# Optimization experiments

Measured on AMD Instinct MI355X. Metric: run time of the kernel, lower is better.

The kernel has to match this reference:

```python
import jax, jax.numpy as jnp
import numpy as np

N_STATE = 64
N_LAYERS = 3


def setup_inputs() -> dict:
    key = jax.random.key(0)
    B, L, D = 8, 8192, 64
    H = 2 * D
    ks = jax.random.split(key, 10)
    x = jax.random.normal(ks[0], (B, L, D), dtype=jnp.float32)
    W_in = jax.random.normal(ks[1], (D, H), dtype=jnp.float32) * 0.05
    b_in = jnp.zeros((H,), jnp.float32)
    # S4D parameterization: dt log-uniform in [1e-3, 1e-1], A = -0.5 + i*pi*n (S4D-Lin init)
    log_dt = jax.random.uniform(ks[2], (N_LAYERS, H), dtype=jnp.float32,
                                minval=float(np.log(1e-3)), maxval=float(np.log(1e-1)))
    log_A_real = jnp.full((N_LAYERS, H, N_STATE), float(np.log(0.5)), jnp.float32)
    A_imag = jnp.tile(jnp.pi * jnp.arange(N_STATE, dtype=jnp.float32), (N_LAYERS, H, 1))
    C_re = jax.random.normal(ks[3], (N_LAYERS, H, N_STATE), dtype=jnp.float32) * (0.5 ** 0.5)
    C_im = jax.random.normal(ks[4], (N_LAYERS, H, N_STATE), dtype=jnp.float32) * (0.5 ** 0.5)
    D_skip = jax.random.normal(ks[5], (N_LAYERS, H), dtype=jnp.float32)
    W_glu = jax.random.normal(ks[6], (N_LAYERS, 2 * H, H), dtype=jnp.float32) * 0.05
    b_glu = jnp.zeros((N_LAYERS, 2 * H), jnp.float32)
    W_out = jax.random.normal(ks[7], (H, D), dtype=jnp.float32) * 0.05
    b_out = jnp.zeros((D,), jnp.float32)
    return {"x": x, "W_in": W_in, "b_in": b_in, "log_dt": log_dt,
            "log_A_real": log_A_real, "A_imag": A_imag, "C_re": C_re, "C_im": C_im,
            "D_skip": D_skip, "W_glu": W_glu, "b_glu": b_glu,
            "W_out": W_out, "b_out": b_out}


def _s4_block(u, log_dt, log_A_real, A_imag, C_re, C_im, D_skip, W_glu, b_glu):
    # u: (B, H, L). S4D: diagonal SSM applied as a long FFT convolution.
    H, L = u.shape[1], u.shape[2]
    dt = jnp.exp(log_dt)[:, None]                       # (H,1)
    A = -jnp.exp(log_A_real) + 1j * A_imag              # (H,N), Re(A)<0 -> stable
    dtA = dt * A                                        # (H,N)
    C = (C_re + 1j * C_im) * jnp.expm1(dtA) / A         # ZOH-discretized C*B
    vand = jnp.exp(dtA[:, :, None] * jnp.arange(L, dtype=jnp.float32))  # (H,N,L)
    K = 2.0 * jnp.einsum('hn,hnl->hl', C, vand).real    # (H,L) SSM kernel
    n = 2 * L
    y = jnp.fft.irfft(jnp.fft.rfft(u, n=n) * jnp.fft.rfft(K, n=n), n=n)[..., :L]
    y = y + u * D_skip[:, None]                         # skip connection D*u
    y = jax.nn.gelu(y)
    z = jnp.einsum('bhl,gh->bgl', y, W_glu) + b_glu[None, :, None]  # pointwise H->2H
    a, g = jnp.split(z, 2, axis=1)
    return a * jax.nn.sigmoid(g)                        # GLU


def _rmsnorm(x):
    # F.normalize(x, dim=-1) * sqrt(dim)
    scale = jnp.sqrt(jnp.asarray(x.shape[-1], jnp.float32))
    nrm = jnp.linalg.norm(x, axis=-1, keepdims=True)
    return x / jnp.maximum(nrm, 1e-12) * scale


def reference(x, W_in, b_in, log_dt, log_A_real, A_imag, C_re, C_im,
              D_skip, W_glu, b_glu, W_out, b_out):
    h = x @ W_in + b_in                                 # (B,L,H)
    for i in range(N_LAYERS):
        u = h.swapaxes(-1, -2)                          # (B,H,L)
        y = _s4_block(u, log_dt[i], log_A_real[i], A_imag[i], C_re[i], C_im[i],
                      D_skip[i], W_glu[i], b_glu[i]).swapaxes(-1, -2)
        h = _rmsnorm(y + h)                             # PreNormResidual
    return h @ W_out + b_out
```

## Files before the change

### kernel.cpp

```cpp
#include <hip/hip_runtime.h>
#include <math.h>

#define BB 8
#define LL 8192
#define DD 64
#define HH 128
#define NN 64
#define NLAYER 3
#define LC 64
#define NC 128
#define LST 137
#define SIS 136

typedef _Float16 half_t;
typedef _Float16 f16x8_t __attribute__((ext_vector_type(8)));
typedef _Float16 f16x4_t __attribute__((ext_vector_type(4)));
typedef _Float16 f16x2_t __attribute__((ext_vector_type(2)));
typedef float    f32x4_t __attribute__((ext_vector_type(4)));

#define SZ_WB   ((size_t)HH*NN*2)
#define SZ_WGT  ((size_t)NLAYER*256*HH/2)
#define SZ_WOT  ((size_t)DD*HH/2)
#define SZ_WIT  ((size_t)HH*DD/2)
#define SZ_AM   ((size_t)HH*64*192/2)
#define SZ_HT   ((size_t)BB*HH*LL/2)
#define SZ_YT   ((size_t)BB*HH*LL/2)

__global__ __launch_bounds__(256) void kPrep(const float* __restrict__ logdt,
   const float* __restrict__ logA, const float* __restrict__ Aim,
   const float* __restrict__ Cre, const float* __restrict__ Cim,
   const float* __restrict__ Wglu, const float* __restrict__ Wout,
   const float* __restrict__ Win,
   float* __restrict__ wb3, float* __restrict__ wl3, half_t* __restrict__ Amat3,
   half_t* __restrict__ wgt, half_t* __restrict__ woT, half_t* __restrict__ wiT) {
  __shared__ float  ktap[4][64];
  __shared__ half_t gst[4][64][128];
  int bid = blockIdx.x;
  int t = threadIdx.x;
  if (bid < 96) {
    int layer = bid >> 5;
    int blk   = bid & 31;
    float* wb = wb3 + (size_t)layer*SZ_WB;
    float* wl = wl3 + (size_t)layer*SZ_WB;
    half_t* Amat = Amat3 + (size_t)layer*HH*64*192;
    int w = t >> 6;
    int n = t & 63;
    int h = blk*4 + w;
    float dt = expf(logdt[layer*HH + h]);
    int idx = (layer*HH + h)*NN + n;
    float ar = -expf(logA[idx]);
    float ai = Aim[idx];
    float er = expf(dt*ar);
    float wr = er*cosf(dt*ai), wi = er*sinf(dt*ai);
    float inv = 1.f/(ar*ar + ai*ai);
    float mr = wr - 1.f, mi = wi;
    float tr = (mr*ar + mi*ai)*inv;
    float ti = (mi*ar - mr*ai)*inv;
    float c0 = Cre[idx], c1 = Cim[idx];
    float cr = c0*tr - c1*ti, ci = c0*ti + c1*tr;
    wb[(h*NN+n)*2] = wr; wb[(h*NN+n)*2+1] = wi;
    float pr = 1.f, pi = 0.f;
    float qr = cr*wr - ci*wi, qi = cr*wi + ci*wr;
    for (int d = 0; d < 64; d++) {
      float kd = cr*pr - ci*pi;
      kd += __shfl_xor(kd, 1);  kd += __shfl_xor(kd, 2);  kd += __shfl_xor(kd, 4);
      kd += __shfl_xor(kd, 8);  kd += __shfl_xor(kd, 16); kd += __shfl_xor(kd, 32);
      if (n == 0) ktap[w][d] = 2.f*kd;
      f16x2_t g2 = { (half_t)(2.f*qr), (half_t)(-2.f*qi) };
      *(f16x2_t*)&gst[w][d][2*n] = g2;
      float npr = pr*wr - pi*wi, npi = pr*wi + pi*wr; pr = npr; pi = npi;
      float nqr = qr*wr - qi*wi, nqi = qr*wi + qi*wr; qr = nqr; qi = nqi;
    }
    wl[(h*NN+n)*2] = pr; wl[(h*NN+n)*2+1] = pi;
    __syncthreads();
    #pragma unroll
    for (int i = 0; i < 16; i++) {
      int idx2 = t + i*256;
      int hh = idx2 >> 10;
      int rem = idx2 & 1023;
      int l = rem >> 4, m8 = rem & 15;
      half_t* Ahh = Amat + (size_t)(blk*4 + hh)*64*192;
      *(f16x8_t*)&Ahh[(size_t)l*192 + 64 + m8*8] = *(const f16x8_t*)&gst[hh][l][m8*8];
    }
    #pragma unroll
    for (int i = 0; i < 8; i++) {
      int idx2 = t + i*256;
      int hh = idx2 >> 9;
      int rem = idx2 & 511;
      int l = rem >> 3, m8 = rem & 7;
      half_t* Ahh = Amat + (size_t)(blk*4 + hh)*64*192;
      f16x8_t v;
      #pragma unroll
      for (int j = 0; j < 8; j++) {
        int m = m8*8 + j;
        v[j] = (half_t)((m <= l) ? ktap[hh][l - m] : 0.f);
      }
      *(f16x8_t*)&Ahh[(size_t)l*192 + m8*8] = v;
    }
  } else if (bid < 144) {
    int tid = (bid - 96)*256 + t;
    const float* src = Wglu + (size_t)tid*8;
    f16x8_t v;
    #pragma unroll
    for (int i = 0; i < 8; i++) v[i] = (half_t)src[i];
    *(f16x8_t*)&wgt[(size_t)tid*8] = v;
  } else if (bid < 176) {
    int tid = (bid - 144)*256 + t;
    int d = tid >> 7, h = tid & 127;
    woT[d*HH + h] = (half_t)Wout[h*DD + d];
  } else {
    int tid = (bid - 176)*256 + t;
    int h = tid >> 6, d = tid & 63;
    wiT[h*DD + d] = (half_t)Win[d*HH + h];
  }
}

__global__ __launch_bounds__(256) void kIn(const float* __restrict__ x,
      const half_t* __restrict__ wiT, const float* __restrict__ bin,
      half_t* __restrict__ hT) {
  __shared__ half_t xs[64*72];
  __shared__ half_t zs[128*72];
  size_t row0 = (size_t)blockIdx.x * 64;
  int t = threadIdx.x;
  #pragma unroll
  for (int i = 0; i < 4; i++) {
    int idx = t + i*256;
    int r = idx >> 4, c4 = idx & 15;
    float4 v = *(const float4*)&x[(row0 + r)*DD + c4*4];
    f16x4_t o = { (half_t)v.x, (half_t)v.y, (half_t)v.z, (half_t)v.w };
    *(f16x4_t*)&xs[r*72 + c4*4] = o;
  }
  __syncthreads();
  int wid = t >> 6, lane = t & 63;
  int lr = lane & 15, lq = lane >> 4, lk = lq*8;
  f32x4_t acc[4][2];
  #pragma unroll
  for (int mr = 0; mr < 4; mr++)
    #pragma unroll
    for (int nc = 0; nc < 2; nc++) {
      float bv = bin[(wid*2 + nc)*16 + lr];
      acc[mr][nc] = (f32x4_t){bv, bv, bv, bv};
    }
  #pragma unroll
  for (int ks = 0; ks < 2; ks++) {
    int k = ks*32 + lk;
    f16x8_t af[4], bf[2];
    #pragma unroll
    for (int mr = 0; mr < 4; mr++) af[mr] = *(const f16x8_t*)&xs[(mr*16 + lr)*72 + k];
    #pragma unroll
    for (int nc = 0; nc < 2; nc++)
      bf[nc] = *(const f16x8_t*)&wiT[(size_t)((wid*2 + nc)*16 + lr)*DD + k];
    #pragma unroll
    for (int mr = 0; mr < 4; mr++)
      #pragma unroll
      for (int nc = 0; nc < 2; nc++)
        acc[mr][nc] = __builtin_amdgcn_mfma_f32_16x16x32_f16(af[mr], bf[nc], acc[mr][nc], 0, 0, 0);
  }
  #pragma unroll
  for (int mr = 0; mr < 4; mr++)
    #pragma unroll
    for (int nc = 0; nc < 2; nc++) {
      int h = (wid*2 + nc)*16 + lr;
      f16x4_t v = { (half_t)acc[mr][nc][0], (half_t)acc[mr][nc][1],
                    (half_t)acc[mr][nc][2], (half_t)acc[mr][nc][3] };
      *(f16x4_t*)&zs[h*72 + mr*16 + lq*4] = v;
    }
  __syncthreads();
  size_t bb = row0 >> 13;
  int l0 = (int)(row0 & 8191);
  int h = t >> 1, hf = t & 1;
  half_t* dst = hT + ((size_t)bb*HH + h)*LL + l0 + hf*32;
  #pragma unroll
  for (int j = 0; j < 4; j++)
    *(f16x8_t*)&dst[j*8] = *(const f16x8_t*)&zs[h*72 + hf*32 + j*8];
}

__global__ __launch_bounds__(512) void kG(const half_t* __restrict__ hT,
      const float* __restrict__ wb, const float* __restrict__ wl,
      const half_t* __restrict__ Amat, half_t* __restrict__ yT) {
  __shared__ half_t va[128*72];
  __shared__ half_t ub[128*72];
  __shared__ half_t spad[128*LST];
  __shared__ float  segT[8*128];
  int t = threadIdx.x;
  int h = blockIdx.x >> 3, b = blockIdx.x & 7;
  {
    int n = t >> 3, q8 = t & 7;
    float wr = wb[(h*NN+n)*2], wi = wb[(h*NN+n)*2+1];
    float ar = wr, ai = wi;
    #pragma unroll
    for (int i = 0; i < 3; i++) { float nr = ar*ar - ai*ai, ni = 2.f*ar*ai; ar = nr; ai = ni; }
    float pr = 1.f, pi = 0.f;
    for (int e = 0; e < 7 - q8; e++) { float nr = pr*ar - pi*ai, ni = pr*ai + pi*ar; pr = nr; pi = ni; }
    int k0 = (7 - q8)*8;
    for (int i = 0; i < 8; i++) {
      int m = 63 - (k0 + i);
      va[(2*n)*72 + m]   = (half_t)pr;
      va[(2*n+1)*72 + m] = (half_t)pi;
      float nr = pr*wr - pi*wi, ni = pr*wi + pi*wr; pr = nr; pi = ni;
    }
  }
  {
    const half_t* src = hT + ((size_t)b*HH + h)*LL;
    #pragma unroll
    for (int i = 0; i < 2; i++) {
      int idx = t + i*512;
      int row = idx >> 3, off = (idx & 7)*8;
      *(f16x8_t*)&ub[row*72 + off] = *(const f16x8_t*)&src[row*64 + off];
    }
  }
  __syncthreads();
  int wid = t >> 6, lane = t & 63;
  int lr = lane & 15, lq = lane >> 4, lk = lq*8;
  {
    int wr_ = wid & 1, wc = wid >> 1;
    f32x4_t acc[4][2];
    #pragma unroll
    for (int mr = 0; mr < 4; mr++) { acc[mr][0] = (f32x4_t){0.f,0.f,0.f,0.f}; acc[mr][1] = (f32x4_t){0.f,0.f,0.f,0.f}; }
    #pragma unroll
    for (int ks = 0; ks < 2; ks++) {
      int k = ks*32 + lk;
      f16x8_t af[4], bf[2];
      #pragma unroll
      for (int mr = 0; mr < 4; mr++) af[mr] = *(const f16x8_t*)&va[(wr_*64 + mr*16 + lr)*72 + k];
      #pragma unroll
      for (int nc = 0; nc < 2; nc++) bf[nc] = *(const f16x8_t*)&ub[(wc*32 + nc*16 + lr)*72 + k];
      #pragma unroll
      for (int mr = 0; mr < 4; mr++)
        #pragma unroll
        for (int nc = 0; nc < 2; nc++)
          acc[mr][nc] = __builtin_amdgcn_mfma_f32_16x16x32_f16(af[mr], bf[nc], acc[mr][nc], 0, 0, 0);
    }
    #pragma unroll
    for (int mr = 0; mr < 4; mr++)
      #pragma unroll
      for (int nc = 0; nc < 2; nc++)
        #pragma unroll
        for (int r = 0; r < 4; r++)
          spad[(wr_*64 + mr*16 + lq*4 + r)*LST + (wc*32 + nc*16 + lr)] = (half_t)acc[mr][nc][r];
  }
  __syncthreads();
  {
    int n = t & 63, seg = t >> 6;
    int c0 = seg*16;
    float w64r = wl[(h*NN+n)*2], w64i = wl[(h*NN+n)*2+1];
    float pregr[16], pregi[16];
    float cr = 0.f, ci = 0.f;
    #pragma unroll
    for (int i = 0; i < 16; i++) {
      int c = c0 + i;
      float lre = (float)spad[(2*n)*LST + c];
      float lim = (float)spad[(2*n+1)*LST + c];
      pregr[i] = cr; pregi[i] = ci;
      float nr = fmaf(w64r, cr, fmaf(-w64i, ci, lre));
      float ni = fmaf(w64i, cr, fmaf(w64r, ci, lim));
      cr = nr; ci = ni;
    }
    segT[seg*128 + 2*n] = cr; segT[seg*128 + 2*n+1] = ci;
    __syncthreads();
    float ar = w64r, ai = w64i;
    #pragma unroll
    for (int i = 0; i < 4; i++) { float nr = ar*ar - ai*ai, ni = 2.f*ar*ai; ar = nr; ai = ni; }
    float br = 0.f, bi = 0.f;
    for (int k = 0; k < seg; k++) {
      float tr_ = segT[k*128 + 2*n], ti_ = segT[k*128 + 2*n+1];
      float nr = fmaf(ar, br, fmaf(-ai, bi, tr_));
      float ni = fmaf(ai, br, fmaf(ar, bi, ti_));
      br = nr; bi = ni;
    }
    float wpr = 1.f, wpi = 0.f;
    #pragma unroll
    for (int i = 0; i < 16; i++) {
      int c = c0 + i;
      float sr = pregr[i] + wpr*br - wpi*bi;
      float si = pregi[i] + wpr*bi + wpi*br;
      f16x2_t v = { (half_t)sr, (half_t)si };
      *(f16x2_t*)&spad[c*SIS + 2*n] = v;
      float nr = wpr*w64r - wpi*w64i, ni = wpr*w64i + wpi*w64r;
      wpr = nr; wpi = ni;
    }
  }
  __syncthreads();
  {
    const half_t* Ag = Amat + (size_t)h*64*192;
    f32x4_t acc[4];
    #pragma unroll
    for (int mr = 0; mr < 4; mr++) acc[mr] = (f32x4_t){0.f,0.f,0.f,0.f};
    int c = wid*16 + lr;
    #pragma unroll
    for (int ks = 0; ks < 6; ks++) {
      int k = ks*32 + lk;
      f16x8_t af[4];
      #pragma unroll
      for (int mr = 0; mr < 4; mr++) af[mr] = *(const f16x8_t*)&Ag[(size_t)(mr*16 + lr)*192 + k];
      f16x8_t bf = (ks < 2) ? *(const f16x8_t*)&ub[c*72 + k]
                            : *(const f16x8_t*)&spad[c*SIS + (k - 64)];
      #pragma unroll
      for (int mr = 0; mr < 4; mr++)
        acc[mr] = __builtin_amdgcn_mfma_f32_16x16x32_f16(af[mr], bf, acc[mr], 0, 0, 0);
    }
    #pragma unroll
    for (int mr = 0; mr < 4; mr++) {
      int l0 = mr*16 + lq*4;
      f16x4_t v = { (half_t)acc[mr][0], (half_t)acc[mr][1],
                    (half_t)acc[mr][2], (half_t)acc[mr][3] };
      *(f16x4_t*)&va[c*72 + l0] = v;
    }
  }
  __syncthreads();
  {
    half_t* yp = yT + ((size_t)b*HH + h)*LL;
    int c = t >> 2, q = t & 3;
    const half_t* src = &va[c*72 + q*16];
    f16x8_t v0 = *(const f16x8_t*)src;
    f16x8_t v1 = *(const f16x8_t*)(src + 8);
    *(f16x8_t*)&yp[c*64 + q*16]     = v0;
    *(f16x8_t*)&yp[c*64 + q*16 + 8] = v1;
  }
}

__global__ __launch_bounds__(512) void kD(const half_t* __restrict__ yT,
     const half_t* __restrict__ hTin, const float* __restrict__ dskip,
     const half_t* __restrict__ wgt, const float* __restrict__ bglu,
     half_t* __restrict__ hT, const half_t* __restrict__ woT,
     const float* __restrict__ bout, float* __restrict__ out, int last) {
  __shared__ half_t ylds[64][136];
  __shared__ half_t ulds[64][136];
  __shared__ float  rpart[8][64];
  size_t row0 = (size_t)blockIdx.x * 64;
  int b  = (int)(row0 >> 13);
  int l0 = (int)(row0 & 8191);
  int t = threadIdx.x;
  int h = t >> 2, q = t & 3;
  int lbase = q*16;
  const half_t* yb  = yT   + ((size_t)b*HH + h)*LL + l0 + lbase;
  const half_t* ubp = hTin + ((size_t)b*HH + h)*LL + l0 + lbase;
  float d = dskip[h];
  #pragma unroll
  for (int j = 0; j < 2; j++) {
    f16x8_t yv = *(const f16x8_t*)&yb[j*8];
    f16x8_t uv = *(const f16x8_t*)&ubp[j*8];
    #pragma unroll
    for (int i = 0; i < 8; i++) {
      float v = fmaf((float)uv[i], d, (float)yv[i]);
      float arg2 = 1.5957691216057308f*(v + 0.044715f*v*v*v);
      arg2 = fminf(fmaxf(arg2, -30.f), 30.f);
      float e = __expf(-arg2);
      float o = v * __builtin_amdgcn_rcpf(1.f + e);
      ylds[lbase + j*8 + i][h] = (half_t)o;
      ulds[lbase + j*8 + i][h] = uv[i];
    }
  }
  __syncthreads();
  {
    int w = t >> 6, lane = t & 63;
    int lr = lane & 15, lq = lane >> 4;
    f32x4_t acc[4][2];
    #pragma unroll
    for (int mt = 0; mt < 4; mt++) { acc[mt][0] = (f32x4_t){0.f,0.f,0.f,0.f}; acc[mt][1] = (f32x4_t){0.f,0.f,0.f,0.f}; }
    #pragma unroll
    for (int ks = 0; ks < 4; ks++) {
      int k = ks*32 + lq*8;
      f16x8_t af[4];
      #pragma unroll
      for (int mt = 0; mt < 4; mt++) af[mt] = *(const f16x8_t*)&ylds[mt*16 + lr][k];
      f16x8_t bfa = *(const f16x8_t*)&wgt[(size_t)(w*16 + lr)*HH + k];
      f16x8_t bfg = *(const f16x8_t*)&wgt[(size_t)((w + 8)*16 + lr)*HH + k];
      #pragma unroll
      for (int mt = 0; mt < 4; mt++) {
        acc[mt][0] = __builtin_amdgcn_mfma_f32_16x16x32_f16(af[mt], bfa, acc[mt][0], 0, 0, 0);
        acc[mt][1] = __builtin_amdgcn_mfma_f32_16x16x32_f16(af[mt], bfg, acc[mt][1], 0, 0, 0);
      }
    }
    __syncthreads();
    int col = w*16 + lr;
    float ba = bglu[col], bg = bglu[col + 128];
    float sp[4][4];
    #pragma unroll
    for (int mt = 0; mt < 4; mt++)
      #pragma unroll
      for (int r = 0; r < 4; r++) {
        int row = mt*16 + lq*4 + r;
        float a = acc[mt][0][r] + ba;
        float g = acc[mt][1][r] + bg;
        float s = __builtin_amdgcn_rcpf(1.f + __expf(-g));
        float z = a*s + (float)ulds[row][col];
        ylds[row][col] = (half_t)z;
        sp[mt][r] = z*z;
      }
    #pragma unroll
    for (int m = 1; m < 16; m <<= 1)
      #pragma unroll
      for (int mt = 0; mt < 4; mt++)
        #pragma unroll
        for (int r = 0; r < 4; r++) sp[mt][r] += __shfl_xor(sp[mt][r], m);
    if (lr == 0) {
      #pragma unroll
      for (int mt = 0; mt < 4; mt++)
        #pragma unroll
        for (int r = 0; r < 4; r++) rpart[w][mt*16 + lq*4 + r] = sp[mt][r];
    }
  }
  __syncthreads();
  f16x8_t o0, o1;
  #pragma unroll
  for (int i = 0; i < 8; i++) {
    int row = lbase + i;
    float rn = rpart[0][row] + rpart[1][row] + rpart[2][row] + rpart[3][row]
             + rpart[4][row] + rpart[5][row] + rpart[6][row] + rpart[7][row];
    float sc = 11.313708498984761f * __builtin_amdgcn_rsqf(fmaxf(rn, 1e-24f));
    o0[i] = (half_t)((float)ylds[row][h]*sc);
  }
  #pragma unroll
  for (int i = 0; i < 8; i++) {
    int row = lbase + 8 + i;
    float rn = rpart[0][row] + rpart[1][row] + rpart[2][row] + rpart[3][row]
             + rpart[4][row] + rpart[5][row] + rpart[6][row] + rpart[7][row];
    float sc = 11.313708498984761f * __builtin_amdgcn_rsqf(fmaxf(rn, 1e-24f));
    o1[i] = (half_t)((float)ylds[row][h]*sc);
  }
  if (!last) {
    half_t* hb = hT + ((size_t)b*HH + h)*LL + l0 + lbase;
    *(f16x8_t*)hb = o0;
    *(f16x8_t*)(hb + 8) = o1;
  } else {
    #pragma unroll
    for (int i = 0; i < 8; i++) ulds[lbase + i][h]     = o0[i];
    #pragma unroll
    for (int i = 0; i < 8; i++) ulds[lbase + 8 + i][h] = o1[i];
    __syncthreads();
    int w = t >> 6, lane = t & 63;
    int lr = lane & 15, lq = lane >> 4;
    int dd = (w & 3)*16 + lr;
    int mth = (w >> 2)*2;
    f32x4_t oacc[2];
    float bv = bout[dd];
    oacc[0] = (f32x4_t){bv, bv, bv, bv};
    oacc[1] = (f32x4_t){bv, bv, bv, bv};
    #pragma unroll
    for (int ks = 0; ks < 4; ks++) {
      int k = ks*32 + lq*8;
      f16x8_t bf = *(const f16x8_t*)&woT[(size_t)dd*HH + k];
      #pragma unroll
      for (int j = 0; j < 2; j++) {
        f16x8_t af2 = *(const f16x8_t*)&ulds[(mth + j)*16 + lr][k];
        oacc[j] = __builtin_amdgcn_mfma_f32_16x16x32_f16(af2, bf, oacc[j], 0, 0, 0);
      }
    }
    #pragma unroll
    for (int j = 0; j < 2; j++)
      #pragma unroll
      for (int r = 0; r < 4; r++)
        out[(row0 + (mth + j)*16 + lq*4 + r)*DD + dd] = oacc[j][r];
  }
}

extern "C" void kernel_launch(void* const* d_in, const int* in_sizes, int n_in,
                              void* d_out, int out_size, void* d_ws, size_t ws_size,
                              hipStream_t stream) {
  const float* x     = (const float*)d_in[0];
  const float* Win   = (const float*)d_in[1];
  const float* bin   = (const float*)d_in[2];
  const float* logdt = (const float*)d_in[3];
  const float* logA  = (const float*)d_in[4];
  const float* Aim   = (const float*)d_in[5];
  const float* Cre   = (const float*)d_in[6];
  const float* Cim   = (const float*)d_in[7];
  const float* Dsk   = (const float*)d_in[8];
  const float* Wglu  = (const float*)d_in[9];
  const float* bglu  = (const float*)d_in[10];
  const float* Wout  = (const float*)d_in[11];
  const float* bout  = (const float*)d_in[12];
  float* out = (float*)d_out;

  float* ws   = (float*)d_ws;
  float* wb3  = ws;
  float* wl3  = wb3 + 3*SZ_WB;
  float* wgtF = wl3 + 3*SZ_WB;
  float* woTF = wgtF + SZ_WGT;
  float* wiTF = woTF + SZ_WOT;
  float* amF  = wiTF + SZ_WIT;
  float* htF  = amF + 3*SZ_AM;
  float* ytF  = htF + SZ_HT;
  half_t* wgt    = (half_t*)wgtF;
  half_t* woT    = (half_t*)woTF;
  half_t* wiT    = (half_t*)wiTF;
  half_t* Amat3  = (half_t*)amF;
  half_t* hT     = (half_t*)htF;
  half_t* yT     = (half_t*)ytF;

  kPrep<<<dim3(208), dim3(256), 0, stream>>>(logdt, logA, Aim, Cre, Cim,
                                             Wglu, Wout, Win,
                                             wb3, wl3, Amat3, wgt, woT, wiT);
  kIn<<<dim3(1024), dim3(256), 0, stream>>>(x, wiT, bin, hT);

  for (int layer = 0; layer < NLAYER; ++layer) {
    const float* wb = wb3 + (size_t)layer*SZ_WB;
    const float* wl = wl3 + (size_t)layer*SZ_WB;
    const half_t* Amat = Amat3 + (size_t)layer*HH*64*192;
    kG<<<dim3(1024), dim3(512), 0, stream>>>(hT, wb, wl, Amat, yT);
    kD<<<dim3(1024), dim3(512), 0, stream>>>(yT, hT, Dsk + layer*HH,
                       wgt + (size_t)layer*256*HH,
                       bglu + layer*2*HH, hT, woT, bout, out,
                       (layer == NLAYER-1) ? 1 : 0);
  }
}
```

Measured before the change: 223.0 us.

## Fuse per-layer kG/kD launches into one persistent cooperative kernel with grid syncs

Replaces the six separate kG and kD launches with a single cooperative persistent kernel. It loops over layers and work-groups and uses grid.sync between stages. Shared memory is carved from one static buffer sized for the larger stage. The aim is to remove kernel launch gaps and tail effects between stages. In exchange it adds grid-wide barriers, caps the grid size by occupancy, and uses a larger static LDS footprint, which may lower occupancy.

```diff
diff --git a/kernel.cpp b/kernel.cpp
--- a/kernel.cpp
+++ b/kernel.cpp
@@ -1,5 +1,8 @@
 #include <hip/hip_runtime.h>
+#include <hip/hip_cooperative_groups.h>
 #include <math.h>
+
+namespace cg = cooperative_groups;
 
 #define BB 8
 #define LL 8192
@@ -7,8 +10,6 @@
 #define HH 128
 #define NN 64
 #define NLAYER 3
-#define LC 64
-#define NC 128
 #define LST 137
 #define SIS 136
 
@@ -175,15 +176,15 @@
     *(f16x8_t*)&dst[j*8] = *(const f16x8_t*)&zs[h*72 + hf*32 + j*8];
 }
 
-__global__ __launch_bounds__(512) void kG(const half_t* __restrict__ hT,
-      const float* __restrict__ wb, const float* __restrict__ wl,
-      const half_t* __restrict__ Amat, half_t* __restrict__ yT) {
-  __shared__ half_t va[128*72];
-  __shared__ half_t ub[128*72];
-  __shared__ half_t spad[128*LST];
-  __shared__ float  segT[8*128];
-  int t = threadIdx.x;
-  int h = blockIdx.x >> 3, b = blockIdx.x & 7;
+__device__ __forceinline__ void kG_body(int wg, int t, char* smem,
+      const half_t* __restrict__ hT, const float* __restrict__ wb,
+      const float* __restrict__ wl, const half_t* __restrict__ Amat,
+      half_t* __restrict__ yT) {
+  half_t* va   = (half_t*)smem;
+  half_t* ub   = (half_t*)(smem + 18432);
+  half_t* spad = (half_t*)(smem + 36864);
+  float*  segT = (float*)(smem + 71936);
+  int h = wg >> 3, b = wg & 7;
   {
     int n = t >> 3, q8 = t & 7;
     float wr = wb[(h*NN+n)*2], wi = wb[(h*NN+n)*2+1];
@@ -319,18 +320,18 @@
   }
 }
 
-__global__ __launch_bounds__(512) void kD(const half_t* __restrict__ yT,
-     const half_t* __restrict__ hTin, const float* __restrict__ dskip,
-     const half_t* __restrict__ wgt, const float* __restrict__ bglu,
-     half_t* __restrict__ hT, const half_t* __restrict__ woT,
-     const float* __restrict__ bout, float* __restrict__ out, int last) {
-  __shared__ half_t ylds[64][136];
-  __shared__ half_t ulds[64][136];
-  __shared__ float  rpart[8][64];
-  size_t row0 = (size_t)blockIdx.x * 64;
+__device__ __forceinline__ void kD_body(int wg, int t, char* smem,
+     const half_t* __restrict__ yT, const half_t* __restrict__ hTin,
+     const float* __restrict__ dskip, const half_t* __restrict__ wgt,
+     const float* __restrict__ bglu, half_t* __restrict__ hT,
+     const half_t* __restrict__ woT, const float* __restrict__ bout,
+     float* __restrict__ out, int last) {
+  half_t* ylds = (half_t*)smem;
+  half_t* ulds = (half_t*)(smem + 17408);
+  float*  rpart = (float*)(smem + 34816);
+  size_t row0 = (size_t)wg * 64;
   int b  = (int)(row0 >> 13);
   int l0 = (int)(row0 & 8191);
-  int t = threadIdx.x;
   int h = t >> 2, q = t & 3;
   int lbase = q*16;
   const half_t* yb  = yT   + ((size_t)b*HH + h)*LL + l0 + lbase;
@@ -347,8 +348,8 @@
       arg2 = fminf(fmaxf(arg2, -30.f), 30.f);
       float e = __expf(-arg2);
       float o = v * __builtin_amdgcn_rcpf(1.f + e);
-      ylds[lbase + j*8 + i][h] = (half_t)o;
-      ulds[lbase + j*8 + i][h] = uv[i];
+      ylds[(lbase + j*8 + i)*136 + h] = (half_t)o;
+      ulds[(lbase + j*8 + i)*136 + h] = uv[i];
     }
   }
   __syncthreads();
@@ -363,7 +364,7 @@
       int k = ks*32 + lq*8;
       f16x8_t af[4];
       #pragma unroll
-      for (int mt = 0; mt < 4; mt++) af[mt] = *(const f16x8_t*)&ylds[mt*16 + lr][k];
+      for (int mt = 0; mt < 4; mt++) af[mt] = *(const f16x8_t*)&ylds[(mt*16 + lr)*136 + k];
       f16x8_t bfa = *(const f16x8_t*)&wgt[(size_t)(w*16 + lr)*HH + k];
       f16x8_t bfg = *(const f16x8_t*)&wgt[(size_t)((w + 8)*16 + lr)*HH + k];
       #pragma unroll
@@ -384,8 +385,8 @@
         float a = acc[mt][0][r] + ba;
         float g = acc[mt][1][r] + bg;
         float s = __builtin_amdgcn_rcpf(1.f + __expf(-g));
-        float z = a*s + (float)ulds[row][col];
-        ylds[row][col] = (half_t)z;
+        float z = a*s + (float)ulds[row*136 + col];
+        ylds[row*136 + col] = (half_t)z;
         sp[mt][r] = z*z;
       }
     #pragma unroll
@@ -398,7 +399,7 @@
       #pragma unroll
       for (int mt = 0; mt < 4; mt++)
         #pragma unroll
-        for (int r = 0; r < 4; r++) rpart[w][mt*16 + lq*4 + r] = sp[mt][r];
+        for (int r = 0; r < 4; r++) rpart[w*64 + mt*16 + lq*4 + r] = sp[mt][r];
     }
   }
   __syncthreads();
@@ -406,18 +407,18 @@
   #pragma unroll
   for (int i = 0; i < 8; i++) {
     int row = lbase + i;
-    float rn = rpart[0][row] + rpart[1][row] + rpart[2][row] + rpart[3][row]
-             + rpart[4][row] + rpart[5][row] + rpart[6][row] + rpart[7][row];
+    float rn = rpart[0*64+row] + rpart[1*64+row] + rpart[2*64+row] + rpart[3*64+row]
+             + rpart[4*64+row] + rpart[5*64+row] + rpart[6*64+row] + rpart[7*64+row];
     float sc = 11.313708498984761f * __builtin_amdgcn_rsqf(fmaxf(rn, 1e-24f));
-    o0[i] = (half_t)((float)ylds[row][h]*sc);
+    o0[i] = (half_t)((float)ylds[row*136 + h]*sc);
   }
   #pragma unroll
   for (int i = 0; i < 8; i++) {
     int row = lbase + 8 + i;
-    float rn = rpart[0][row] + rpart[1][row] + rpart[2][row] + rpart[3][row]
-             + rpart[4][row] + rpart[5][row] + rpart[6][row] + rpart[7][row];
+    float rn = rpart[0*64+row] + rpart[1*64+row] + rpart[2*64+row] + rpart[3*64+row]
+             + rpart[4*64+row] + rpart[5*64+row] + rpart[6*64+row] + rpart[7*64+row];
     float sc = 11.313708498984761f * __builtin_amdgcn_rsqf(fmaxf(rn, 1e-24f));
-    o1[i] = (half_t)((float)ylds[row][h]*sc);
+    o1[i] = (half_t)((float)ylds[row*136 + h]*sc);
   }
   if (!last) {
     half_t* hb = hT + ((size_t)b*HH + h)*LL + l0 + lbase;
@@ -425,9 +426,9 @@
     *(f16x8_t*)(hb + 8) = o1;
   } else {
     #pragma unroll
-    for (int i = 0; i < 8; i++) ulds[lbase + i][h]     = o0[i];
-    #pragma unroll
-    for (int i = 0; i < 8; i++) ulds[lbase + 8 + i][h] = o1[i];
+    for (int i = 0; i < 8; i++) ulds[(lbase + i)*136 + h]     = o0[i];
+    #pragma unroll
+    for (int i = 0; i < 8; i++) ulds[(lbase + 8 + i)*136 + h] = o1[i];
     __syncthreads();
     int w = t >> 6, lane = t & 63;
     int lr = lane & 15, lq = lane >> 4;
@@ -443,7 +444,7 @@
       f16x8_t bf = *(const f16x8_t*)&woT[(size_t)dd*HH + k];
       #pragma unroll
       for (int j = 0; j < 2; j++) {
-        f16x8_t af2 = *(const f16x8_t*)&ulds[(mth + j)*16 + lr][k];
+        f16x8_t af2 = *(const f16x8_t*)&ulds[((mth + j)*16 + lr)*136 + k];
         oacc[j] = __builtin_amdgcn_mfma_f32_16x16x32_f16(af2, bf, oacc[j], 0, 0, 0);
       }
     }
@@ -452,6 +453,35 @@
       #pragma unroll
       for (int r = 0; r < 4; r++)
         out[(row0 + (mth + j)*16 + lq*4 + r)*DD + dd] = oacc[j][r];
+  }
+}
+
+__global__ __launch_bounds__(512) void kLayers(
+      half_t* hT, half_t* yT,
+      const float* wb3, const float* wl3, const half_t* Amat3,
+      const half_t* wgt, const float* Dsk, const float* bglu,
+      const half_t* woT, const float* bout, float* out) {
+  cg::grid_group grid = cg::this_grid();
+  __shared__ __align__(16) char smem[76032];
+  int t = threadIdx.x;
+  for (int layer = 0; layer < NLAYER; ++layer) {
+    const float* wb = wb3 + (size_t)layer*SZ_WB;
+    const float* wl = wl3 + (size_t)layer*SZ_WB;
+    const half_t* Amat = Amat3 + (size_t)layer*HH*64*192;
+    for (int wg = blockIdx.x; wg < 1024; wg += gridDim.x) {
+      kG_body(wg, t, smem, hT, wb, wl, Amat, yT);
+      __syncthreads();
+    }
+    grid.sync();
+    const half_t* wgl = wgt + (size_t)layer*256*HH;
+    const float* dskl = Dsk + layer*HH;
+    const float* bgl  = bglu + layer*2*HH;
+    int last = (layer == NLAYER-1) ? 1 : 0;
+    for (int wg = blockIdx.x; wg < 1024; wg += gridDim.x) {
+      kD_body(wg, t, smem, yT, hT, dskl, wgl, bgl, hT, woT, bout, out, last);
+      __syncthreads();
+    }
+    grid.sync();
   }
 }
 
@@ -494,14 +524,17 @@
                                              wb3, wl3, Amat3, wgt, woT, wiT);
   kIn<<<dim3(1024), dim3(256), 0, stream>>>(x, wiT, bin, hT);
 
-  for (int layer = 0; layer < NLAYER; ++layer) {
-    const float* wb = wb3 + (size_t)layer*SZ_WB;
-    const float* wl = wl3 + (size_t)layer*SZ_WB;
-    const half_t* Amat = Amat3 + (size_t)layer*HH*64*192;
-    kG<<<dim3(1024), dim3(512), 0, stream>>>(hT, wb, wl, Amat, yT);
-    kD<<<dim3(1024), dim3(512), 0, stream>>>(yT, hT, Dsk + layer*HH,
-                       wgt + (size_t)layer*256*HH,
-                       bglu + layer*2*HH, hT, woT, bout, out,
-                       (layer == NLAYER-1) ? 1 : 0);
-  }
+  int occ = 0;
+  hipOccupancyMaxActiveBlocksPerMultiprocessor(&occ, (const void*)kLayers, 512, 0);
+  if (occ < 1) occ = 1;
+  int grid = occ * 256;
+  if (grid > 512) grid = 512;
+  const float* wb3c = wb3; const float* wl3c = wl3;
+  const half_t* am3c = Amat3; const half_t* wgtc = wgt;
+  const half_t* woTc = woT; const float* boutc = bout;
+  const float* dskc = Dsk; const float* bgluc = bglu;
+  void* args[] = { (void*)&hT, (void*)&yT, (void*)&wb3c, (void*)&wl3c, (void*)&am3c,
+                   (void*)&wgtc, (void*)&dskc, (void*)&bgluc, (void*)&woTc,
+                   (void*)&boutc, (void*)&out };
+  hipLaunchCooperativeKernel((void*)kLayers, dim3(grid), dim3(512), args, 0, stream);
 }
```

Measured after the change: 474.8 us. +112.9%, slower.
